# Performance work log

Measured on AMD Instinct MI355X. Metric: run time of the kernel, lower is better.

The kernel has to match this reference:

```python
import jax, jax.numpy as jnp
import numpy as np

B, T = 64, 512
V, E, H, L = 100000, 256, 256, 9


def _lstm(x, Wx, Wh, b):
    # x: [B,T,E] -> hs: [B,T,H]; Keras gate order i,f,c,o
    xg = jnp.einsum('bte,eg->btg', x, Wx) + b  # [B,T,4H]
    h0 = jnp.zeros((x.shape[0], Wh.shape[0]), x.dtype)

    def step(carry, xt):
        h, c = carry
        g = xt + h @ Wh
        i, f, gc, o = jnp.split(g, 4, axis=-1)
        c = jax.nn.sigmoid(f) * c + jax.nn.sigmoid(i) * jnp.tanh(gc)
        h = jax.nn.sigmoid(o) * jnp.tanh(c)
        return (h, c), h

    _, hs = jax.lax.scan(step, (h0, h0), jnp.swapaxes(xg, 0, 1))
    return jnp.swapaxes(hs, 0, 1)


def _crf_log_likelihood(logits, tags, seq_len, trans):
    # logits: [B,T,L], tags: [B,T] int, seq_len: [B] int, trans: [L,L]
    Bb, Tt, Ll = logits.shape
    t_idx = jnp.arange(Tt)
    mask = (t_idx[None, :] < seq_len[:, None]).astype(logits.dtype)  # [B,T]
    # gold path score: unary + pairwise transitions
    unary = jnp.take_along_axis(logits, tags[..., None], axis=-1)[..., 0]  # [B,T]
    unary_score = jnp.sum(unary * mask, axis=-1)
    binary = trans[tags[:, :-1], tags[:, 1:]]  # [B,T-1]
    binary_score = jnp.sum(binary * mask[:, 1:], axis=-1)
    score = unary_score + binary_score
    # forward algorithm (log partition)
    alpha0 = logits[:, 0]  # [B,L]
    step_mask = t_idx[1:, None] < seq_len[None, :]  # [T-1,B]

    def step(alpha, xs):
        logit_t, m = xs  # [B,L], [B]
        new = jax.nn.logsumexp(alpha[:, :, None] + trans[None], axis=1) + logit_t
        alpha = jnp.where(m[:, None], new, alpha)
        return alpha, None

    alpha, _ = jax.lax.scan(step, alpha0, (jnp.swapaxes(logits[:, 1:], 0, 1), step_mask))
    log_norm = jax.nn.logsumexp(alpha, axis=-1)  # [B]
    return score - log_norm


def setup_inputs() -> dict:
    key = jax.random.key(0)
    ks = jax.random.split(key, 12)
    s = 0.05
    return {
        'tokens': jax.random.randint(ks[0], (B, T), 0, V),
        'labels': jax.random.randint(ks[1], (B, T), 0, L),
        'emb_table': jax.random.normal(ks[2], (V, E), jnp.float32) * s,
        'Wx_f': jax.random.normal(ks[3], (E, 4 * H), jnp.float32) * s,
        'Wh_f': jax.random.normal(ks[4], (H, 4 * H), jnp.float32) * s,
        'b_f': jnp.zeros((4 * H,), jnp.float32),
        'Wx_b': jax.random.normal(ks[5], (E, 4 * H), jnp.float32) * s,
        'Wh_b': jax.random.normal(ks[6], (H, 4 * H), jnp.float32) * s,
        'b_b': jnp.zeros((4 * H,), jnp.float32),
        'W_dense': jax.random.normal(ks[7], (2 * H, L), jnp.float32) * s,
        'b_dense': jnp.zeros((L,), jnp.float32),
        'trans': jax.random.uniform(ks[8], (L, L), jnp.float32),
    }


def reference(tokens, labels, emb_table, Wx_f, Wh_f, b_f, Wx_b, Wh_b, b_b, W_dense, b_dense, trans):
    # seq_len = count of non-pad (nonzero) tokens, as in the original call()
    seq_len = jnp.sum((tokens != 0).astype(jnp.int32), axis=-1)  # [B]
    emb = emb_table[tokens]  # [B,T,E]  (dropout inactive at inference)
    h_fwd = _lstm(emb, Wx_f, Wh_f, b_f)
    h_bwd = _lstm(emb[:, ::-1], Wx_b, Wh_b, b_b)[:, ::-1]
    enc = jnp.concatenate([h_fwd, h_bwd], axis=-1)  # [B,T,2H]
    logits = enc @ W_dense + b_dense  # [B,T,L]
    ll = _crf_log_likelihood(logits, labels, seq_len, trans)  # [B]
    return logits, seq_len, ll
```

## Files before the change

### kernel.cpp

```cpp
#include <hip/hip_runtime.h>
#include <hip/hip_fp16.h>


typedef unsigned int  uint32;
typedef unsigned short ushort16;
typedef unsigned long long uint64;
typedef __attribute__((ext_vector_type(8))) short  short8;
typedef __attribute__((ext_vector_type(4))) float  floatx4;
typedef __attribute__((ext_vector_type(2))) _Float16 half2t;

#define BB 64
#define TT 512
#define NT (BB*TT)
#define G4 1024
#define NL 9

__device__ inline float bf2f(ushort16 u) {
  return __builtin_bit_cast(float, ((uint32)u) << 16);
}
__device__ inline ushort16 f2bf(float f) {
  uint32 u = __builtin_bit_cast(uint32, f);
  u += 0x7fffu + ((u >> 16) & 1u);
  return (ushort16)(u >> 16);
}
__device__ inline float sigf(float x)  { return 1.0f / (1.0f + __expf(-x)); }
__device__ inline float tanhf_(float x){ return 1.0f - 2.0f / (1.0f + __expf(2.0f * x)); }

__device__ inline float fdot2_(uint32 w, half2t h, float acc) {
  return __builtin_amdgcn_fdot2(__builtin_bit_cast(half2t, w), h, acc, false);
}

__global__ __launch_bounds__(64) void k_seqlen(const int* __restrict__ tokens,
                                               int* __restrict__ slen,
                                               float* __restrict__ out_sl) {
  const int b = blockIdx.x, lane = threadIdx.x;
  int cnt = 0;
  for (int t = lane; t < TT; t += 64) cnt += (tokens[b * TT + t] != 0) ? 1 : 0;
  #pragma unroll
  for (int off = 32; off >= 1; off >>= 1) cnt += __shfl_down(cnt, off, 64);
  if (lane == 0) { slen[b] = cnt; out_sl[b] = (float)cnt; }
}

__global__ __launch_bounds__(256) void k_embed(const int* __restrict__ tokens,
                                               const float* __restrict__ emb,
                                               ushort16* __restrict__ A) {
  const int f = blockIdx.x * 256 + threadIdx.x;
  const int e = f * 4;
  const int row = e >> 8;
  const int col = e & 255;
  const int tok = tokens[row];
  const float4 v = *(const float4*)(emb + (size_t)tok * 256 + col);
  uint32 lo = (uint32)f2bf(v.x) | ((uint32)f2bf(v.y) << 16);
  uint32 hi = (uint32)f2bf(v.z) | ((uint32)f2bf(v.w) << 16);
  *(uint2*)(A + e) = make_uint2(lo, hi);
}

__global__ __launch_bounds__(256) void k_wxprep(const float* __restrict__ Wxf,
                                                const float* __restrict__ Wxb,
                                                ushort16* __restrict__ BT) {
  const int id = blockIdx.x * 256 + threadIdx.x;
  const int c = id >> 8, k = id & 255;
  const float v = (c < G4) ? Wxf[k * G4 + c] : Wxb[k * G4 + (c - G4)];
  BT[c * 256 + k] = f2bf(v);
}

__global__ __launch_bounds__(256) void k_whprep(const float* __restrict__ Wh,
                                                uint32* __restrict__ W2) {
  const int id = blockIdx.x * 256 + threadIdx.x;
  const int k2 = id >> 10, c = id & 1023;
  const float w0 = Wh[(2 * k2) * G4 + c];
  const float w1 = Wh[(2 * k2 + 1) * G4 + c];
  const ushort16 b0 = __builtin_bit_cast(ushort16, (_Float16)w0);
  const ushort16 b1 = __builtin_bit_cast(ushort16, (_Float16)w1);
  W2[id] = ((uint32)b1 << 16) | (uint32)b0;
}

__global__ __launch_bounds__(256) void k_gemm_xg(const ushort16* __restrict__ A,
                                                 const ushort16* __restrict__ BT,
                                                 const float* __restrict__ bias_f,
                                                 const float* __restrict__ bias_b,
                                                 ushort16* __restrict__ xgf,
                                                 ushort16* __restrict__ xgb) {
  __shared__ __align__(16) ushort16 As[64 * 36];
  __shared__ __align__(16) ushort16 Bs[64 * 36];
  const int m0 = blockIdx.x * 64;
  const int n0 = blockIdx.y * 64;
  const int tid = threadIdx.x;
  const int wave = tid >> 6, lane = tid & 63;
  const int lr = tid >> 2;
  const int lc = (tid & 3) * 8;
  const int am = lane & 15, aq = lane >> 4;
  floatx4 acc[4];
  #pragma unroll
  for (int j = 0; j < 4; ++j) acc[j] = (floatx4){0.f, 0.f, 0.f, 0.f};

  for (int k0 = 0; k0 < 256; k0 += 32) {
    const uint4 va = *(const uint4*)(A  + ((m0 + lr) * 256 + k0 + lc));
    const uint4 vb = *(const uint4*)(BT + ((n0 + lr) * 256 + k0 + lc));
    *(uint2*)&As[lr * 36 + lc]     = make_uint2(va.x, va.y);
    *(uint2*)&As[lr * 36 + lc + 4] = make_uint2(va.z, va.w);
    *(uint2*)&Bs[lr * 36 + lc]     = make_uint2(vb.x, vb.y);
    *(uint2*)&Bs[lr * 36 + lc + 4] = make_uint2(vb.z, vb.w);
    __syncthreads();
    union { uint2 u[2]; short8 s; } fa, fb;
    fa.u[0] = *(const uint2*)&As[(wave * 16 + am) * 36 + aq * 8];
    fa.u[1] = *(const uint2*)&As[(wave * 16 + am) * 36 + aq * 8 + 4];
    #pragma unroll
    for (int j = 0; j < 4; ++j) {
      fb.u[0] = *(const uint2*)&Bs[(j * 16 + am) * 36 + aq * 8];
      fb.u[1] = *(const uint2*)&Bs[(j * 16 + am) * 36 + aq * 8 + 4];
      acc[j] = __builtin_amdgcn_mfma_f32_16x16x32_bf16(fa.s, fb.s, acc[j], 0, 0, 0);
    }
    __syncthreads();
  }
  const int orow = m0 + wave * 16 + aq * 4;
  #pragma unroll
  for (int j = 0; j < 4; ++j) {
    const int col = n0 + j * 16 + am;
    const float bv = (col < G4) ? bias_f[col] : bias_b[col - G4];
    #pragma unroll
    for (int r = 0; r < 4; ++r) {
      const float v = acc[j][r] + bv;
      const int row = orow + r;
      if (col < G4) xgf[row * G4 + col] = f2bf(v);
      else          xgb[row * G4 + (col - G4)] = f2bf(v);
    }
  }
}

__global__ __launch_bounds__(256) void k_zero(uint64* __restrict__ xh) {
  xh[blockIdx.x * 256 + threadIdx.x] = 0ull;
}

__global__ __launch_bounds__(512, 2) void k_lstm(const ushort16* __restrict__ xgf,
                                                 const ushort16* __restrict__ xgb,
                                                 const uint32* __restrict__ Whf,
                                                 const uint32* __restrict__ Whb,
                                                 uint64* __restrict__ xh,
                                                 float* __restrict__ enc) {
  __shared__ __align__(16) uint32 h2[2][128];
  __shared__ float gl[512];
  const int bid  = blockIdx.x;
  const int dir  = bid >> 7;
  const int b    = (bid >> 1) & 63;
  const int half = bid & 1;
  const int tid  = threadIdx.x;
  const int w = tid >> 6, l = tid & 63;
  const int q = tid >> 7, r = tid & 127;
  const int col = q * 256 + half * 128 + r;
  const ushort16* __restrict__ xg = dir ? xgb : xgf;
  const uint32* __restrict__ W2   = dir ? Whb : Whf;
  uint64* const xmine = xh + ((size_t)bid << 7);
  const uint64* const xpeer = xh + ((size_t)(bid ^ 1) << 7);

  const int ownBase  = half * 64;
  const int peerBase = 64 - ownBase;
  uint32 wv[128];
  #pragma unroll
  for (int i = 0; i < 64; ++i) wv[i]      = W2[(ownBase  + i) * 1024 + col];
  #pragma unroll
  for (int i = 0; i < 64; ++i) wv[64 + i] = W2[(peerBase + i) * 1024 + col];
  #pragma unroll
  for (int i = 0; i < 128; ++i) asm volatile("" : "+v"(wv[i]));

  if (tid < 128) { h2[0][tid] = 0u; }
  float c_state = 0.f;
  __syncthreads();

  const int t0 = dir ? (TT - 1) : 0;
  ushort16 xA = xg[(size_t)(b * TT + t0) * G4 + col];

  for (int s = 0; s < TT; ++s) {
    const int par = s & 1;
    if (w == 0 && s > 0) {
      const uint32 want = (uint32)s;
      uint64 v;
      for (;;) {
        v = __hip_atomic_load(xpeer + (par << 6) + l,
                              __ATOMIC_RELAXED, __HIP_MEMORY_SCOPE_AGENT);
        if (__all((uint32)(v >> 32) == want)) break;
        __builtin_amdgcn_s_sleep(2);
      }
      h2[par][64 + l] = (uint32)v;
    }
    float a0 = bf2f(xA), a1 = 0.f, a2 = 0.f, a3 = 0.f;
    if (s + 1 < TT) {
      const int t1 = dir ? (TT - 2 - s) : (s + 1);
      xA = xg[(size_t)(b * TT + t1) * G4 + col];
    }
    const uint4* hb = (const uint4*)h2[par];
    #pragma unroll
    for (int blk = 0; blk < 16; ++blk) {
      const uint4 hq = hb[blk];
      a0 = fdot2_(wv[blk * 4 + 0], __builtin_bit_cast(half2t, hq.x), a0);
      a1 = fdot2_(wv[blk * 4 + 1], __builtin_bit_cast(half2t, hq.y), a1);
      a2 = fdot2_(wv[blk * 4 + 2], __builtin_bit_cast(half2t, hq.z), a2);
      a3 = fdot2_(wv[blk * 4 + 3], __builtin_bit_cast(half2t, hq.w), a3);
    }
    __syncthreads();
    #pragma unroll
    for (int blk = 16; blk < 32; ++blk) {
      const uint4 hq = hb[blk];
      a0 = fdot2_(wv[blk * 4 + 0], __builtin_bit_cast(half2t, hq.x), a0);
      a1 = fdot2_(wv[blk * 4 + 1], __builtin_bit_cast(half2t, hq.y), a1);
      a2 = fdot2_(wv[blk * 4 + 2], __builtin_bit_cast(half2t, hq.z), a2);
      a3 = fdot2_(wv[blk * 4 + 3], __builtin_bit_cast(half2t, hq.w), a3);
    }
    gl[tid] = (a0 + a1) + (a2 + a3);
    __syncthreads();
    if (tid < 128) {
      const float gi = gl[tid];
      const float gf = gl[128 + tid];
      const float gg = gl[256 + tid];
      const float go = gl[384 + tid];
      c_state = sigf(gf) * c_state + sigf(gi) * tanhf_(gg);
      const float h = sigf(go) * tanhf_(c_state);
      const int t = dir ? (TT - 1 - s) : s;
      enc[(size_t)(b * TT + t) * 512 + dir * 256 + half * 128 + tid] = h;
      const int hv = (int)(uint32)__builtin_bit_cast(ushort16, (_Float16)h);
      const int ho = __shfl_xor(hv, 1, 64);
      if (!(tid & 1)) {
        const uint32 pk = ((uint32)hv & 0xffffu) | ((uint32)ho << 16);
        h2[par ^ 1][tid >> 1] = pk;
        if (s + 1 < TT) {
          const uint64 pv = ((uint64)(uint32)(s + 1) << 32) | (uint64)pk;
          __hip_atomic_store(xmine + ((par ^ 1) << 6) + (tid >> 1), pv,
                             __ATOMIC_RELAXED, __HIP_MEMORY_SCOPE_AGENT);
        }
      }
    }
    __syncthreads();
  }
}

__global__ __launch_bounds__(256) void k_dense(const float* __restrict__ enc,
                                               const float* __restrict__ Wd,
                                               const float* __restrict__ bd,
                                               float* __restrict__ logits) {
  __shared__ float Wl[512 * NL];
  __shared__ float bl[NL];
  const int tid = threadIdx.x;
  for (int i = tid; i < 512 * NL; i += 256) Wl[i] = Wd[i];
  if (tid < NL) bl[tid] = bd[tid];
  __syncthreads();
  const int wave = tid >> 6, lane = tid & 63;
  const int row = blockIdx.x * 4 + wave;
  const float* er = enc + (size_t)row * 512;
  float p[NL];
  #pragma unroll
  for (int c = 0; c < NL; ++c) p[c] = 0.f;
  #pragma unroll
  for (int u = 0; u < 8; ++u) {
    const int k = u * 64 + lane;
    const float v = er[k];
    const float* wr = &Wl[k * NL];
    #pragma unroll
    for (int c = 0; c < NL; ++c) p[c] += v * wr[c];
  }
  #pragma unroll
  for (int c = 0; c < NL; ++c) {
    #pragma unroll
    for (int off = 32; off >= 1; off >>= 1) p[c] += __shfl_down(p[c], off, 64);
  }
  if (lane == 0) {
    float* orow = logits + (size_t)row * NL;
    #pragma unroll
    for (int c = 0; c < NL; ++c) orow[c] = p[c] + bl[c];
  }
}

__global__ __launch_bounds__(64) void k_crf(const float* __restrict__ logits,
                                            const int* __restrict__ labels,
                                            const int* __restrict__ slen,
                                            const float* __restrict__ trans,
                                            float* __restrict__ out_ll) {
  __shared__ float tr[NL * NL];
  __shared__ float alpha[NL];
  const int b = blockIdx.x;
  const int lane = threadIdx.x;
  for (int i = lane; i < NL * NL; i += 64) tr[i] = trans[i];
  __syncthreads();
  const int len = slen[b];
  const int* tg = labels + b * TT;
  const float* lg = logits + (size_t)b * TT * NL;
  float s = 0.f;
  for (int t = lane; t < TT; t += 64)
    if (t < len) s += lg[t * NL + tg[t]];
  for (int t = lane; t < TT - 1; t += 64)
    if (t + 1 < len) s += tr[tg[t] * NL + tg[t + 1]];
  #pragma unroll
  for (int off = 32; off >= 1; off >>= 1) s += __shfl_down(s, off, 64);
  if (lane < NL) alpha[lane] = lg[lane];
  __syncthreads();
  if (lane < NL) {
    const int j = lane;
    for (int t = 1; t < TT; ++t) {
      if (t < len) {
        float av[NL];
        float m = -1e30f;
        #pragma unroll
        for (int i = 0; i < NL; ++i) { av[i] = alpha[i] + tr[i * NL + j]; m = fmaxf(m, av[i]); }
        float ss = 0.f;
        #pragma unroll
        for (int i = 0; i < NL; ++i) ss += __expf(av[i] - m);
        const float nj = m + __logf(ss) + lg[t * NL + j];
        alpha[j] = nj;
      }
    }
  }
  __syncthreads();
  if (lane == 0) {
    float m = -1e30f;
    #pragma unroll
    for (int i = 0; i < NL; ++i) m = fmaxf(m, alpha[i]);
    float ss = 0.f;
    #pragma unroll
    for (int i = 0; i < NL; ++i) ss += __expf(alpha[i] - m);
    out_ll[b] = s - (m + __logf(ss));
  }
}

extern "C" void kernel_launch(void* const* d_in, const int* in_sizes, int n_in,
                              void* d_out, int out_size, void* d_ws, size_t ws_size,
                              hipStream_t stream) {
  (void)in_sizes; (void)n_in; (void)out_size; (void)ws_size;
  const int*   tokens = (const int*)d_in[0];
  const int*   labels = (const int*)d_in[1];
  const float* emb    = (const float*)d_in[2];
  const float* Wxf    = (const float*)d_in[3];
  const float* Whf    = (const float*)d_in[4];
  const float* bf_    = (const float*)d_in[5];
  const float* Wxb    = (const float*)d_in[6];
  const float* Whb    = (const float*)d_in[7];
  const float* bb_    = (const float*)d_in[8];
  const float* Wd     = (const float*)d_in[9];
  const float* bd     = (const float*)d_in[10];
  const float* trans  = (const float*)d_in[11];
  float* out = (float*)d_out;

  char* ws = (char*)d_ws;
  ushort16* A    = (ushort16*)(ws + 0);
  ushort16* BT   = (ushort16*)(ws + 16777216);
  uint32*   W2f  = (uint32*)  (ws + 17825792);
  uint32*   W2b  = (uint32*)  (ws + 18350080);
  ushort16* xgf  = (ushort16*)(ws + 18874368);
  ushort16* xgb  = (ushort16*)(ws + 85983232);
  float*    enc  = (float*)   (ws + 153092096);
  int*      slen = (int*)     (ws + 220200960);
  uint64*   xh   = (uint64*)  (ws + 0);

  k_seqlen<<<BB, 64, 0, stream>>>(tokens, slen, out + NT * NL);
  k_embed <<<NT * 256 / 4 / 256, 256, 0, stream>>>(tokens, emb, A);
  k_wxprep<<<2048 * 256 / 256, 256, 0, stream>>>(Wxf, Wxb, BT);
  k_whprep<<<128 * 1024 / 256, 256, 0, stream>>>(Whf, W2f);
  k_whprep<<<128 * 1024 / 256, 256, 0, stream>>>(Whb, W2b);
  k_gemm_xg<<<dim3(NT / 64, 2048 / 64), 256, 0, stream>>>(A, BT, bf_, bb_, xgf, xgb);
  k_zero  <<<128, 256, 0, stream>>>(xh);
  k_lstm  <<<256, 512, 0, stream>>>(xgf, xgb, W2f, W2b, xh, enc);
  k_dense <<<NT / 4, 256, 0, stream>>>(enc, Wd, bd, out);
  k_crf   <<<BB, 64, 0, stream>>>(out, labels, slen, trans, out + NT * NL + BB);
}
```

Measured before the change: 1.354 ms.

## Batch 16 sequences per LSTM block and use MFMA for recurrent matmul

The recurrent LSTM kernel now processes 16 batch rows per block pair, with 16 blocks in total instead of 256. The h·Wh product is computed with 16x16x32 f16 MFMA instructions in place of per-column fdot2 chains. Input gate projections are staged through LDS one step ahead, and the peer-block h exchange now carries a full 16-row tile per step. This cuts redundant weight-register work per sequence but leaves only 16 CUs busy, so each step's latency relies on MFMA throughput and a larger cross-block handshake.

```diff
diff --git a/kernel.cpp b/kernel.cpp
--- a/kernel.cpp
+++ b/kernel.cpp
@@ -6,14 +6,16 @@
 typedef unsigned short ushort16;
 typedef unsigned long long uint64;
 typedef __attribute__((ext_vector_type(8))) short  short8;
+typedef __attribute__((ext_vector_type(8))) _Float16 half8;
 typedef __attribute__((ext_vector_type(4))) float  floatx4;
-typedef __attribute__((ext_vector_type(2))) _Float16 half2t;
 
 #define BB 64
 #define TT 512
 #define NT (BB*TT)
 #define G4 1024
 #define NL 9
+#define GSTR 18
+#define XSTR 522
 
 __device__ inline float bf2f(ushort16 u) {
   return __builtin_bit_cast(float, ((uint32)u) << 16);
@@ -25,9 +27,10 @@
 }
 __device__ inline float sigf(float x)  { return 1.0f / (1.0f + __expf(-x)); }
 __device__ inline float tanhf_(float x){ return 1.0f - 2.0f / (1.0f + __expf(2.0f * x)); }
-
-__device__ inline float fdot2_(uint32 w, half2t h, float acc) {
-  return __builtin_amdgcn_fdot2(__builtin_bit_cast(half2t, w), h, acc, false);
+__device__ inline uint32 f16pk(float lo, float hi) {
+  const uint32 a = (uint32)__builtin_bit_cast(ushort16, (_Float16)lo);
+  const uint32 b = (uint32)__builtin_bit_cast(ushort16, (_Float16)hi);
+  return a | (b << 16);
 }
 
 __global__ __launch_bounds__(64) void k_seqlen(const int* __restrict__ tokens,
@@ -138,95 +141,154 @@
                                                  const uint32* __restrict__ Whb,
                                                  uint64* __restrict__ xh,
                                                  float* __restrict__ enc) {
-  __shared__ __align__(16) uint32 h2[2][128];
-  __shared__ float gl[512];
+  __shared__ __align__(16) uint32 haf[2][2048];
+  __shared__ __align__(16) float  gT[512 * GSTR];
+  __shared__ __align__(16) ushort16 xl[2][16 * XSTR];
   const int bid  = blockIdx.x;
-  const int dir  = bid >> 7;
-  const int b    = (bid >> 1) & 63;
+  const int dir  = bid >> 3;
+  const int grp  = (bid >> 1) & 3;
   const int half = bid & 1;
   const int tid  = threadIdx.x;
   const int w = tid >> 6, l = tid & 63;
-  const int q = tid >> 7, r = tid & 127;
-  const int col = q * 256 + half * 128 + r;
+  const int n = l & 15, aq = l >> 4;
   const ushort16* __restrict__ xg = dir ? xgb : xgf;
   const uint32* __restrict__ W2   = dir ? Whb : Whf;
-  uint64* const xmine = xh + ((size_t)bid << 7);
-  const uint64* const xpeer = xh + ((size_t)(bid ^ 1) << 7);
-
-  const int ownBase  = half * 64;
-  const int peerBase = 64 - ownBase;
-  uint32 wv[128];
-  #pragma unroll
-  for (int i = 0; i < 64; ++i) wv[i]      = W2[(ownBase  + i) * 1024 + col];
-  #pragma unroll
-  for (int i = 0; i < 64; ++i) wv[64 + i] = W2[(peerBase + i) * 1024 + col];
-  #pragma unroll
-  for (int i = 0; i < 128; ++i) asm volatile("" : "+v"(wv[i]));
-
-  if (tid < 128) { h2[0][tid] = 0u; }
-  float c_state = 0.f;
+  uint64* const xmine = xh + ((size_t)bid << 11);
+  const uint64* const xpeer = xh + ((size_t)(bid ^ 1) << 11);
+
+  const int qg = w >> 1;
+  const int gcolbase = qg * 256 + half * 128 + (w & 1) * 64 + n;
+  uint4 wq[32];
+  #pragma unroll
+  for (int j = 0; j < 4; ++j) {
+    const int gcol = gcolbase + j * 16;
+    #pragma unroll
+    for (int kk = 0; kk < 8; ++kk) {
+      const int kb = (kk < 4) ? (half * 64 + kk * 16)
+                              : ((1 - half) * 64 + (kk - 4) * 16);
+      union { uint32 u[4]; uint4 v; } t_;
+      #pragma unroll
+      for (int d = 0; d < 4; ++d)
+        t_.u[d] = W2[(size_t)(kb + aq * 4 + d) * 1024 + gcol];
+      wq[j * 8 + kk] = t_.v;
+    }
+  }
+  #pragma unroll
+  for (int i = 0; i < 32; ++i)
+    asm volatile("" : "+v"(wq[i].x), "+v"(wq[i].y), "+v"(wq[i].z), "+v"(wq[i].w));
+
+  const int m_nl = (tid >> 1) & 15;
+  const int u0   = (tid >> 5) * 8 + (tid & 1) * 4;
+  const int p0   = u0 >> 1;
+  const int m_pl = tid & 15;
+  const int pp0  = (tid >> 4) * 2;
+  const int haf_pl = ((4 + (pp0 >> 4)) * 64 + ((pp0 >> 2) & 3) * 16 + m_pl) * 4
+                   + (pp0 & 3);
+  const int srow = tid >> 5;
+  const int slc  = (tid & 31) * 16;
+  const size_t sgoff = (size_t)((slc >> 7) * 256 + half * 128 + (slc & 127));
+  const int batch0 = grp * 16;
+
+  float c0 = 0.f, c1 = 0.f, c2 = 0.f, c3 = 0.f;
+
+  *(uint4*)&haf[0][tid * 4] = make_uint4(0u, 0u, 0u, 0u);
+  {
+    const int ts = dir ? (TT - 1) : 0;
+    const ushort16* src = xg + ((size_t)((batch0 + srow) * TT + ts)) * G4 + sgoff;
+    const uint4 x0 = *(const uint4*)src;
+    const uint4 x1 = *(const uint4*)(src + 8);
+    uint32* dst = (uint32*)&xl[0][srow * XSTR + slc];
+    dst[0] = x0.x; dst[1] = x0.y; dst[2] = x0.z; dst[3] = x0.w;
+    dst[4] = x1.x; dst[5] = x1.y; dst[6] = x1.z; dst[7] = x1.w;
+  }
   __syncthreads();
-
-  const int t0 = dir ? (TT - 1) : 0;
-  ushort16 xA = xg[(size_t)(b * TT + t0) * G4 + col];
 
   for (int s = 0; s < TT; ++s) {
     const int par = s & 1;
-    if (w == 0 && s > 0) {
+    uint4 x0, x1;
+    const bool do_stage = (s + 1 < TT);
+    if (do_stage) {
+      const int ts1 = dir ? (TT - 2 - s) : (s + 1);
+      const ushort16* src = xg + ((size_t)((batch0 + srow) * TT + ts1)) * G4 + sgoff;
+      x0 = *(const uint4*)src;
+      x1 = *(const uint4*)(src + 8);
+    }
+    floatx4 a0 = {0.f,0.f,0.f,0.f}, a1 = {0.f,0.f,0.f,0.f};
+    floatx4 a2 = {0.f,0.f,0.f,0.f}, a3 = {0.f,0.f,0.f,0.f};
+    const uint32* hafp = haf[par];
+    #pragma unroll
+    for (int kk = 0; kk < 4; ++kk) {
+      const half8 av = *(const half8*)(hafp + kk * 256 + l * 4);
+      a0 = __builtin_amdgcn_mfma_f32_16x16x32_f16(av, __builtin_bit_cast(half8, wq[ 0 + kk]), a0, 0, 0, 0);
+      a1 = __builtin_amdgcn_mfma_f32_16x16x32_f16(av, __builtin_bit_cast(half8, wq[ 8 + kk]), a1, 0, 0, 0);
+      a2 = __builtin_amdgcn_mfma_f32_16x16x32_f16(av, __builtin_bit_cast(half8, wq[16 + kk]), a2, 0, 0, 0);
+      a3 = __builtin_amdgcn_mfma_f32_16x16x32_f16(av, __builtin_bit_cast(half8, wq[24 + kk]), a3, 0, 0, 0);
+    }
+    if (s > 0) {
+      const uint64* src = xpeer + (size_t)par * 1024 + m_pl * 64 + pp0;
       const uint32 want = (uint32)s;
-      uint64 v;
+      uint64 v0, v1;
       for (;;) {
-        v = __hip_atomic_load(xpeer + (par << 6) + l,
-                              __ATOMIC_RELAXED, __HIP_MEMORY_SCOPE_AGENT);
-        if (__all((uint32)(v >> 32) == want)) break;
-        __builtin_amdgcn_s_sleep(2);
+        v0 = __hip_atomic_load(src,     __ATOMIC_RELAXED, __HIP_MEMORY_SCOPE_AGENT);
+        v1 = __hip_atomic_load(src + 1, __ATOMIC_RELAXED, __HIP_MEMORY_SCOPE_AGENT);
+        if (__all(((uint32)(v0 >> 32) == want) && ((uint32)(v1 >> 32) == want))) break;
+        __builtin_amdgcn_s_sleep(1);
       }
-      h2[par][64 + l] = (uint32)v;
-    }
-    float a0 = bf2f(xA), a1 = 0.f, a2 = 0.f, a3 = 0.f;
-    if (s + 1 < TT) {
-      const int t1 = dir ? (TT - 2 - s) : (s + 1);
-      xA = xg[(size_t)(b * TT + t1) * G4 + col];
-    }
-    const uint4* hb = (const uint4*)h2[par];
-    #pragma unroll
-    for (int blk = 0; blk < 16; ++blk) {
-      const uint4 hq = hb[blk];
-      a0 = fdot2_(wv[blk * 4 + 0], __builtin_bit_cast(half2t, hq.x), a0);
-      a1 = fdot2_(wv[blk * 4 + 1], __builtin_bit_cast(half2t, hq.y), a1);
-      a2 = fdot2_(wv[blk * 4 + 2], __builtin_bit_cast(half2t, hq.z), a2);
-      a3 = fdot2_(wv[blk * 4 + 3], __builtin_bit_cast(half2t, hq.w), a3);
+      *(uint2*)&haf[par][haf_pl] = make_uint2((uint32)v0, (uint32)v1);
+    }
+    if (do_stage) {
+      uint32* dst = (uint32*)&xl[par ^ 1][srow * XSTR + slc];
+      dst[0] = x0.x; dst[1] = x0.y; dst[2] = x0.z; dst[3] = x0.w;
+      dst[4] = x1.x; dst[5] = x1.y; dst[6] = x1.z; dst[7] = x1.w;
     }
     __syncthreads();
     #pragma unroll
-    for (int blk = 16; blk < 32; ++blk) {
-      const uint4 hq = hb[blk];
-      a0 = fdot2_(wv[blk * 4 + 0], __builtin_bit_cast(half2t, hq.x), a0);
-      a1 = fdot2_(wv[blk * 4 + 1], __builtin_bit_cast(half2t, hq.y), a1);
-      a2 = fdot2_(wv[blk * 4 + 2], __builtin_bit_cast(half2t, hq.z), a2);
-      a3 = fdot2_(wv[blk * 4 + 3], __builtin_bit_cast(half2t, hq.w), a3);
-    }
-    gl[tid] = (a0 + a1) + (a2 + a3);
+    for (int kk = 4; kk < 8; ++kk) {
+      const half8 av = *(const half8*)(hafp + kk * 256 + l * 4);
+      a0 = __builtin_amdgcn_mfma_f32_16x16x32_f16(av, __builtin_bit_cast(half8, wq[ 0 + kk]), a0, 0, 0, 0);
+      a1 = __builtin_amdgcn_mfma_f32_16x16x32_f16(av, __builtin_bit_cast(half8, wq[ 8 + kk]), a1, 0, 0, 0);
+      a2 = __builtin_amdgcn_mfma_f32_16x16x32_f16(av, __builtin_bit_cast(half8, wq[16 + kk]), a2, 0, 0, 0);
+      a3 = __builtin_amdgcn_mfma_f32_16x16x32_f16(av, __builtin_bit_cast(half8, wq[24 + kk]), a3, 0, 0, 0);
+    }
+    {
+      const int cb = (qg * 128 + (w & 1) * 64 + n) * GSTR + aq * 4;
+      *(float2*)&gT[cb +  0 * GSTR] = make_float2(a0[0], a0[1]);
+      *(float2*)&gT[cb +  0 * GSTR + 2] = make_float2(a0[2], a0[3]);
+      *(float2*)&gT[cb + 16 * GSTR] = make_float2(a1[0], a1[1]);
+      *(float2*)&gT[cb + 16 * GSTR + 2] = make_float2(a1[2], a1[3]);
+      *(float2*)&gT[cb + 32 * GSTR] = make_float2(a2[0], a2[1]);
+      *(float2*)&gT[cb + 32 * GSTR + 2] = make_float2(a2[2], a2[3]);
+      *(float2*)&gT[cb + 48 * GSTR] = make_float2(a3[0], a3[1]);
+      *(float2*)&gT[cb + 48 * GSTR + 2] = make_float2(a3[2], a3[3]);
+    }
     __syncthreads();
-    if (tid < 128) {
-      const float gi = gl[tid];
-      const float gf = gl[128 + tid];
-      const float gg = gl[256 + tid];
-      const float go = gl[384 + tid];
-      c_state = sigf(gf) * c_state + sigf(gi) * tanhf_(gg);
-      const float h = sigf(go) * tanhf_(c_state);
-      const int t = dir ? (TT - 1 - s) : s;
-      enc[(size_t)(b * TT + t) * 512 + dir * 256 + half * 128 + tid] = h;
-      const int hv = (int)(uint32)__builtin_bit_cast(ushort16, (_Float16)h);
-      const int ho = __shfl_xor(hv, 1, 64);
-      if (!(tid & 1)) {
-        const uint32 pk = ((uint32)hv & 0xffffu) | ((uint32)ho << 16);
-        h2[par ^ 1][tid >> 1] = pk;
-        if (s + 1 < TT) {
-          const uint64 pv = ((uint64)(uint32)(s + 1) << 32) | (uint64)pk;
-          __hip_atomic_store(xmine + ((par ^ 1) << 6) + (tid >> 1), pv,
-                             __ATOMIC_RELAXED, __HIP_MEMORY_SCOPE_AGENT);
-        }
+    {
+      const int ts = dir ? (TT - 1 - s) : s;
+      const ushort16* xr = &xl[par][m_nl * XSTR];
+      float h[4];
+      #pragma unroll
+      for (int j = 0; j < 4; ++j) {
+        const int u = u0 + j;
+        const float pi = gT[(0 * 128 + u) * GSTR + m_nl] + bf2f(xr[0 * 128 + u]);
+        const float pf = gT[(1 * 128 + u) * GSTR + m_nl] + bf2f(xr[1 * 128 + u]);
+        const float pg = gT[(2 * 128 + u) * GSTR + m_nl] + bf2f(xr[2 * 128 + u]);
+        const float po = gT[(3 * 128 + u) * GSTR + m_nl] + bf2f(xr[3 * 128 + u]);
+        float& c = (j == 0) ? c0 : (j == 1) ? c1 : (j == 2) ? c2 : c3;
+        c = sigf(pf) * c + sigf(pi) * tanhf_(pg);
+        h[j] = sigf(po) * tanhf_(c);
+      }
+      *(float4*)&enc[((size_t)((batch0 + m_nl) * TT + ts)) * 512
+                     + dir * 256 + half * 128 + u0] = *(float4*)h;
+      const uint32 pk0 = f16pk(h[0], h[1]);
+      const uint32 pk1 = f16pk(h[2], h[3]);
+      *(uint2*)&haf[par ^ 1][tid * 2] = make_uint2(pk0, pk1);
+      if (s + 1 < TT) {
+        const uint64 tagv = ((uint64)(uint32)(s + 1)) << 32;
+        uint64* dst = xmine + (size_t)(par ^ 1) * 1024 + m_nl * 64 + p0;
+        __hip_atomic_store(dst,     tagv | (uint64)pk0,
+                           __ATOMIC_RELAXED, __HIP_MEMORY_SCOPE_AGENT);
+        __hip_atomic_store(dst + 1, tagv | (uint64)pk1,
+                           __ATOMIC_RELAXED, __HIP_MEMORY_SCOPE_AGENT);
       }
     }
     __syncthreads();
@@ -356,7 +418,7 @@
   k_whprep<<<128 * 1024 / 256, 256, 0, stream>>>(Whb, W2b);
   k_gemm_xg<<<dim3(NT / 64, 2048 / 64), 256, 0, stream>>>(A, BT, bf_, bb_, xgf, xgb);
   k_zero  <<<128, 256, 0, stream>>>(xh);
-  k_lstm  <<<256, 512, 0, stream>>>(xgf, xgb, W2f, W2b, xh, enc);
+  k_lstm  <<<16, 512, 0, stream>>>(xgf, xgb, W2f, W2b, xh, enc);
   k_dense <<<NT / 4, 256, 0, stream>>>(enc, Wd, bd, out);
   k_crf   <<<BB, 64, 0, stream>>>(out, labels, slen, trans, out + NT * NL + BB);
 }
```

Measured after the change: 2.017 ms. +49.0%, slower.
